# Kernel tuning notes

Hardware: AMD Instinct MI355X
Metric: run time of the kernel (lower is better)

Reference implementation:

```python
import jax, jax.numpy as jnp
import numpy as np

EXPERTS, IN_DIM, OUT_DIM, BATCH = 8, 1024, 1024, 16384

def setup_inputs() -> dict:
    key = jax.random.key(0)
    k1, k2, k3, k4 = jax.random.split(key, 4)
    bound = np.sqrt(6.0 / (IN_DIM * OUT_DIM)).astype(np.float32)
    bbound = np.sqrt(6.0 / (1 * OUT_DIM)).astype(np.float32)
    return {
        "x": jax.random.normal(k1, (BATCH, IN_DIM), dtype=jnp.float32),
        "weights": jax.random.uniform(k2, (BATCH, EXPERTS), dtype=jnp.float32),
        "W": jax.random.uniform(k3, (EXPERTS, IN_DIM, OUT_DIM), jnp.float32, -bound, bound),
        "b": jax.random.uniform(k4, (EXPERTS, 1, OUT_DIM), jnp.float32, -bbound, bbound),
    }

def reference(x, weights, W, b):
    # y[b,o] = sum_e weights[b,e] * (x[b,:] @ W[e] + b[e])
    # Fused triple einsum avoids materializing the [B,E,O] intermediate.
    y = jnp.einsum("be,bi,eio->bo", weights, x, W)
    y = y + jnp.einsum("be,eo->bo", weights, b[:, 0, :])
    return y
```

## Files before the change

### kernel.cpp

```cpp
#include <hip/hip_runtime.h>
#include <hip/hip_bf16.h>
#include <stdint.h>

#define BATCH   16384
#define EXPERTS 8
#define IN_DIM  1024
#define OUT_DIM 1024

typedef unsigned short u16;
typedef short  bf16x8 __attribute__((ext_vector_type(8)));
typedef float  f32x4  __attribute__((ext_vector_type(4)));

__device__ __forceinline__ u16 f2bf(float f) {
  uint32_t u = __float_as_uint(f);
  u += 0x7fffu + ((u >> 16) & 1u);
  return (u16)(u >> 16);
}

#define GLDS16(g, l)                                                      \
  __builtin_amdgcn_global_load_lds(                                       \
      (const __attribute__((address_space(1))) void*)(g),                 \
      (__attribute__((address_space(3))) void*)(l), 16, 0, 0)

#define MFMA_BF16 __builtin_amdgcn_mfma_f32_16x16x32_bf16
#define SB0 __builtin_amdgcn_sched_barrier(0)
#define LGKM(N) asm volatile("s_waitcnt lgkmcnt(" #N ")" ::: "memory")
#define VM0     asm volatile("s_waitcnt vmcnt(0)" ::: "memory")

__global__ void cvt_x(const float* __restrict__ x, u16* __restrict__ xb) {
  size_t i = ((size_t)blockIdx.x * 256 + threadIdx.x) * 4;
  float4 v = *reinterpret_cast<const float4*>(x + i);
  ushort4 o;
  o.x = f2bf(v.x); o.y = f2bf(v.y); o.z = f2bf(v.z); o.w = f2bf(v.w);
  *reinterpret_cast<ushort4*>(xb + i) = o;
}

__global__ void cvt_w(const float* __restrict__ W, u16* __restrict__ wbt) {
  __shared__ u16 t[64][72];
  const int e  = blockIdx.z;
  const int i0 = blockIdx.x * 64;
  const int o0 = blockIdx.y * 64;
  const int tid = threadIdx.x;
  const int c  = (tid & 15) * 4;
  const int r_ = tid >> 4;
  const float* src = W + ((size_t)e << 20);
#pragma unroll
  for (int p = 0; p < 4; ++p) {
    int r = r_ + p * 16;
    float4 v = *reinterpret_cast<const float4*>(src + (size_t)(i0 + r) * 1024 + o0 + c);
    t[r][c + 0] = f2bf(v.x); t[r][c + 1] = f2bf(v.y);
    t[r][c + 2] = f2bf(v.z); t[r][c + 3] = f2bf(v.w);
  }
  __syncthreads();
  u16* dst = wbt + ((size_t)e << 20);
#pragma unroll
  for (int p = 0; p < 4; ++p) {
    int orow = r_ + p * 16;
    ushort4 u;
    u.x = t[c + 0][orow]; u.y = t[c + 1][orow];
    u.z = t[c + 2][orow]; u.w = t[c + 3][orow];
    *reinterpret_cast<ushort4*>(dst + (size_t)(o0 + orow) * 1024 + i0 + c) = u;
  }
}

__global__ __launch_bounds__(512, 2)
void zgemm(const u16* __restrict__ xb, const u16* __restrict__ wbt,
           const float* __restrict__ wts, const float* __restrict__ bias,
           float* __restrict__ y) {
  __shared__ u16 sm[69632];
  char* smb = (char*)sm;
  float* rl = (float*)(sm + 65536);

  const int tid = threadIdx.x;
  const int l   = tid & 63;
  const int w   = tid >> 6;
  const int wm  = w >> 2;
  const int wn  = w & 3;
  const int x8  = blockIdx.x & 7;
  const int jj  = blockIdx.x >> 3;
  const int b0  = ((x8 << 3) + (jj >> 2)) << 8;
  const int n0  = (jj & 3) << 8;

#pragma unroll
  for (int i = 0; i < 4; ++i) {
    const int flat = tid + i * 512;
    const int e = flat & 7, r = flat >> 3;
    const float* wr = wts + (size_t)(b0 + r) * EXPERTS;
    float we = fmaxf(wr[e], 1e-20f);
    float rr = (e < 7) ? we / fmaxf(wr[e + 1], 1e-20f) : we;
    rl[e * 256 + r] = rr;
  }

  const int rbl   = (w << 3) + (l >> 3);
  const int chunk = ((l & 7) ^ (l >> 3)) << 3;
  const u16* pAg = xb  + (size_t)(b0 + rbl) * IN_DIM + chunk;
  const u16* pBg = wbt + (size_t)(n0 + rbl) * 1024 + chunk;

  const int l15  = l & 15;
  const int kb0  = (((l >> 4) << 4)) ^ ((l & 7) << 4);
  const int arow = (wm * 128 + l15) * 128;
  const int brow = (wn * 64 + l15) * 128;
  const int wlo  = (wm << 9) + ((l >> 4) << 4);

  f32x4 acc[8][4];
#pragma unroll
  for (int m = 0; m < 8; ++m)
#pragma unroll
    for (int n = 0; n < 4; ++n) acc[m][n] = (f32x4){0.f, 0.f, 0.f, 0.f};

#define STG_A(q, dstE, kv)                                                 \
  GLDS16(pAg + (size_t)((q) * 64) * 1024 + (size_t)(kv) * 64,              \
         sm + (dstE) + (q) * 4096 + (w << 9))
#define STG_B(q, dstE, off)                                                \
  GLDS16(pBg + (off) + (size_t)((q) * 64) * 1024,                          \
         sm + (dstE) + (q) * 4096 + (w << 9))

#define MM(AV, BV, MB)                                                     \
  __builtin_amdgcn_s_setprio(1);                                           \
  _Pragma("unroll")                                                        \
  for (int m = 0; m < 4; ++m)                                              \
    _Pragma("unroll")                                                      \
    for (int n = 0; n < 4; ++n)                                            \
      acc[(MB) + m][n] = MFMA_BF16(AV[m], BV[n], acc[(MB) + m][n], 0, 0, 0); \
  __builtin_amdgcn_s_setprio(0);

  STG_A(0, 0, 0); STG_A(1, 0, 0); STG_A(2, 0, 0); STG_A(3, 0, 0);
  STG_B(0, 32768, 0); STG_B(1, 32768, 0); STG_B(2, 32768, 0); STG_B(3, 32768, 0);
  VM0;
  LGKM(0);
  __builtin_amdgcn_s_barrier();

#define BODY(TT, ARB, BRB, AWE, BWE)                                       \
  {                                                                        \
    const int tn  = ((TT) + 1) & 127;                                      \
    const int e1  = tn >> 4, k1 = tn & 15;                                 \
    const size_t boffg = (size_t)e1 * 1048576 + (size_t)k1 * 64;           \
    bf16x8 a0[4], b0v[4], a1[4], a2v[4], b1v[4], a3[4];                    \
    _Pragma("unroll")                                                      \
    for (int m = 0; m < 4; ++m)                                            \
      a0[m] = *(const bf16x8*)(smb + (ARB) + arow + m * 2048 + kb0);       \
    _Pragma("unroll")                                                      \
    for (int n = 0; n < 4; ++n)                                            \
      b0v[n] = *(const bf16x8*)(smb + (BRB) + brow + n * 2048 + kb0);      \
    _Pragma("unroll")                                                      \
    for (int m = 0; m < 4; ++m)                                            \
      a1[m] = *(const bf16x8*)(smb + (ARB) + arow + (m + 4) * 2048 + kb0); \
    STG_A(0, AWE, k1); STG_A(1, AWE, k1); STG_A(2, AWE, k1); STG_A(3, AWE, k1); \
    STG_B(0, BWE, boffg); STG_B(1, BWE, boffg);                            \
    STG_B(2, BWE, boffg); STG_B(3, BWE, boffg);                            \
    LGKM(4); SB0;                              \
    _Pragma("unroll")                                                      \
    for (int m = 0; m < 4; ++m)                                            \
      a2v[m] = *(const bf16x8*)(smb + (ARB) + arow + m * 2048 + (kb0 ^ 64)); \
    _Pragma("unroll")                                                      \
    for (int n = 0; n < 4; ++n)                                            \
      b1v[n] = *(const bf16x8*)(smb + (BRB) + brow + n * 2048 + (kb0 ^ 64)); \
    MM(a0, b0v, 0)                                                 \
    LGKM(8); SB0;                                             \
    _Pragma("unroll")                                                      \
    for (int m = 0; m < 4; ++m)                                            \
      a3[m] = *(const bf16x8*)(smb + (ARB) + arow + (m + 4) * 2048 + (kb0 ^ 64)); \
    MM(a1, b0v, 4)                                                 \
    LGKM(4); SB0;                                             \
    MM(a2v, b1v, 0)                                                \
    LGKM(0); SB0;                                             \
    MM(a3, b1v, 4)                                                 \
    VM0;                                           \
    __builtin_amdgcn_s_barrier();              \
    if (((TT) & 15) == 15 && (TT) != 127) {                                \
      const int e = (TT) >> 4;                                             \
      f32x4 rv[8];                                                         \
      _Pragma("unroll")                                                    \
      for (int m = 0; m < 8; ++m)                                          \
        rv[m] = *(const f32x4*)(smb + 131072 + e * 1024 + wlo + m * 64);   \
      LGKM(0); SB0;                                                        \
      _Pragma("unroll")                                                    \
      for (int m = 0; m < 8; ++m)                                          \
        _Pragma("unroll")                                                  \
        for (int n = 0; n < 4; ++n) acc[m][n] *= rv[m];                    \
    }                                                                      \
  }

#pragma unroll 1
  for (int t = 0; t < 128; t += 2) {
    BODY(t,     0,     65536, 16384, 49152)
    BODY(t + 1, 32768, 98304, 0,     32768)
  }
  VM0; LGKM(0);

  float bv[4][8];
#pragma unroll
  for (int n = 0; n < 4; ++n) {
    const int c = n0 + wn * 64 + n * 16 + l15;
#pragma unroll
    for (int ee = 0; ee < 8; ++ee) bv[n][ee] = bias[ee * OUT_DIM + c];
  }
#pragma unroll
  for (int m = 0; m < 8; ++m) {
    const f32x4 rv7 = *(const f32x4*)(smb + 131072 + 7 * 1024 + wlo + m * 64);
    const int r0 = b0 + wm * 128 + m * 16 + ((l >> 4) << 2);
#pragma unroll
    for (int j = 0; j < 4; ++j) {
      const float* wr = wts + (size_t)(r0 + j) * EXPERTS;
      float w8[8];
#pragma unroll
      for (int ee = 0; ee < 8; ++ee) w8[ee] = wr[ee];
#pragma unroll
      for (int n = 0; n < 4; ++n) {
        const int c = n0 + wn * 64 + n * 16 + l15;
        float v = acc[m][n][j] * rv7[j];
#pragma unroll
        for (int ee = 0; ee < 8; ++ee) v += w8[ee] * bv[n][ee];
        y[(size_t)(r0 + j) * OUT_DIM + c] = v;
      }
    }
  }
}

extern "C" void kernel_launch(void* const* d_in, const int* in_sizes, int n_in,
                              void* d_out, int out_size, void* d_ws, size_t ws_size,
                              hipStream_t stream) {
  const float* x    = (const float*)d_in[0];
  const float* wts  = (const float*)d_in[1];
  const float* W    = (const float*)d_in[2];
  const float* bias = (const float*)d_in[3];
  float* y = (float*)d_out;

  const size_t xb_elems = (size_t)BATCH * IN_DIM;
  const size_t wb_elems = (size_t)EXPERTS * IN_DIM * OUT_DIM;
  if (ws_size < (xb_elems + wb_elems) * sizeof(u16)) return;
  u16* xb  = (u16*)d_ws;
  u16* wbt = xb + xb_elems;

  cvt_x<<<(BATCH * IN_DIM) / (4 * 256), 256, 0, stream>>>(x, xb);
  cvt_w<<<dim3(IN_DIM / 64, OUT_DIM / 64, EXPERTS), 256, 0, stream>>>(W, wbt);
  zgemm<<<dim3(256), 512, 0, stream>>>(xb, wbt, wts, bias, y);
}
```

Measured before the change: 243.8 us.

## Switch main GEMM from 16x16x32 to 32x32x16 bf16 MFMA tiles

Replaces the 16x16x32 MFMA with 32x32x16 MFMA, regrouping each warp's 128x64 tile into 4x2 blocks of 32x32 accumulators. This changes the LDS fragment reads (fewer B reads per k-step) and the per-expert rescale and epilogue index mapping. The epilogue also loads the eight routing weights with two float4 loads instead of scalar loads. The intent is to cut LDS traffic and instruction count per FLOP, at the cost of a different LDS-wait schedule and new swizzle and index arithmetic that must still line up with the staging layout.

```diff
diff --git a/kernel.cpp b/kernel.cpp
--- a/kernel.cpp
+++ b/kernel.cpp
@@ -10,6 +10,7 @@
 typedef unsigned short u16;
 typedef short  bf16x8 __attribute__((ext_vector_type(8)));
 typedef float  f32x4  __attribute__((ext_vector_type(4)));
+typedef float  f32x16 __attribute__((ext_vector_type(16)));
 
 __device__ __forceinline__ u16 f2bf(float f) {
   uint32_t u = __float_as_uint(f);
@@ -22,7 +23,7 @@
       (const __attribute__((address_space(1))) void*)(g),                 \
       (__attribute__((address_space(3))) void*)(l), 16, 0, 0)
 
-#define MFMA_BF16 __builtin_amdgcn_mfma_f32_16x16x32_bf16
+#define MFMA32 __builtin_amdgcn_mfma_f32_32x32x16_bf16
 #define SB0 __builtin_amdgcn_sched_barrier(0)
 #define LGKM(N) asm volatile("s_waitcnt lgkmcnt(" #N ")" ::: "memory")
 #define VM0     asm volatile("s_waitcnt vmcnt(0)" ::: "memory")
@@ -96,17 +97,19 @@
   const u16* pAg = xb  + (size_t)(b0 + rbl) * IN_DIM + chunk;
   const u16* pBg = wbt + (size_t)(n0 + rbl) * 1024 + chunk;
 
-  const int l15  = l & 15;
-  const int kb0  = (((l >> 4) << 4)) ^ ((l & 7) << 4);
-  const int arow = (wm * 128 + l15) * 128;
-  const int brow = (wn * 64 + l15) * 128;
-  const int wlo  = (wm << 9) + ((l >> 4) << 4);
-
-  f32x4 acc[8][4];
-#pragma unroll
-  for (int m = 0; m < 8; ++m)
-#pragma unroll
-    for (int n = 0; n < 4; ++n) acc[m][n] = (f32x4){0.f, 0.f, 0.f, 0.f};
+  const int l31   = l & 31;
+  const int kb0   = ((l >> 5) << 4) ^ ((l & 7) << 4);
+  const int arow2 = (wm * 128 + l31) * 128;
+  const int brow2 = (wn * 64 + l31) * 128;
+  const int wlo2  = (wm << 9) + ((l >> 5) << 4);
+
+  f32x16 acc[4][2];
+#pragma unroll
+  for (int mb = 0; mb < 4; ++mb)
+#pragma unroll
+    for (int nb = 0; nb < 2; ++nb)
+#pragma unroll
+      for (int j = 0; j < 16; ++j) acc[mb][nb][j] = 0.f;
 
 #define STG_A(q, dstE, kv)                                                 \
   GLDS16(pAg + (size_t)((q) * 64) * 1024 + (size_t)(kv) * 64,              \
@@ -115,13 +118,21 @@
   GLDS16(pBg + (off) + (size_t)((q) * 64) * 1024,                          \
          sm + (dstE) + (q) * 4096 + (w << 9))
 
-#define MM(AV, BV, MB)                                                     \
+#define RDF(AS, BS, KB, ARB, BRB)                                          \
+    _Pragma("unroll")                                                      \
+    for (int mb = 0; mb < 4; ++mb)                                         \
+      AS[mb] = *(const bf16x8*)(smb + (ARB) + arow2 + mb * 4096 + (KB));   \
+    _Pragma("unroll")                                                      \
+    for (int nb = 0; nb < 2; ++nb)                                         \
+      BS[nb] = *(const bf16x8*)(smb + (BRB) + brow2 + nb * 4096 + (KB));
+
+#define MM32(AV, BV)                                                       \
   __builtin_amdgcn_s_setprio(1);                                           \
   _Pragma("unroll")                                                        \
-  for (int m = 0; m < 4; ++m)                                              \
+  for (int mb = 0; mb < 4; ++mb)                                           \
     _Pragma("unroll")                                                      \
-    for (int n = 0; n < 4; ++n)                                            \
-      acc[(MB) + m][n] = MFMA_BF16(AV[m], BV[n], acc[(MB) + m][n], 0, 0, 0); \
+    for (int nb = 0; nb < 2; ++nb)                                         \
+      acc[mb][nb] = MFMA32(AV[mb], BV[nb], acc[mb][nb], 0, 0, 0);          \
   __builtin_amdgcn_s_setprio(0);
 
   STG_A(0, 0, 0); STG_A(1, 0, 0); STG_A(2, 0, 0); STG_A(3, 0, 0);
@@ -135,49 +146,43 @@
     const int tn  = ((TT) + 1) & 127;                                      \
     const int e1  = tn >> 4, k1 = tn & 15;                                 \
     const size_t boffg = (size_t)e1 * 1048576 + (size_t)k1 * 64;           \
-    bf16x8 a0[4], b0v[4], a1[4], a2v[4], b1v[4], a3[4];                    \
-    _Pragma("unroll")                                                      \
-    for (int m = 0; m < 4; ++m)                                            \
-      a0[m] = *(const bf16x8*)(smb + (ARB) + arow + m * 2048 + kb0);       \
-    _Pragma("unroll")                                                      \
-    for (int n = 0; n < 4; ++n)                                            \
-      b0v[n] = *(const bf16x8*)(smb + (BRB) + brow + n * 2048 + kb0);      \
-    _Pragma("unroll")                                                      \
-    for (int m = 0; m < 4; ++m)                                            \
-      a1[m] = *(const bf16x8*)(smb + (ARB) + arow + (m + 4) * 2048 + kb0); \
+    bf16x8 A0[4], B0[2], A1[4], B1[2], A2[4], B2[2], A3[4], B3[2];         \
+    RDF(A0, B0, kb0,      ARB, BRB)                                        \
+    RDF(A1, B1, kb0 ^ 32, ARB, BRB)                                        \
     STG_A(0, AWE, k1); STG_A(1, AWE, k1); STG_A(2, AWE, k1); STG_A(3, AWE, k1); \
     STG_B(0, BWE, boffg); STG_B(1, BWE, boffg);                            \
     STG_B(2, BWE, boffg); STG_B(3, BWE, boffg);                            \
-    LGKM(4); SB0;                              \
-    _Pragma("unroll")                                                      \
-    for (int m = 0; m < 4; ++m)                                            \
-      a2v[m] = *(const bf16x8*)(smb + (ARB) + arow + m * 2048 + (kb0 ^ 64)); \
-    _Pragma("unroll")                                                      \
-    for (int n = 0; n < 4; ++n)                                            \
-      b1v[n] = *(const bf16x8*)(smb + (BRB) + brow + n * 2048 + (kb0 ^ 64)); \
-    MM(a0, b0v, 0)                                                 \
-    LGKM(8); SB0;                                             \
-    _Pragma("unroll")                                                      \
-    for (int m = 0; m < 4; ++m)                                            \
-      a3[m] = *(const bf16x8*)(smb + (ARB) + arow + (m + 4) * 2048 + (kb0 ^ 64)); \
-    MM(a1, b0v, 4)                                                 \
-    LGKM(4); SB0;                                             \
-    MM(a2v, b1v, 0)                                                \
+    LGKM(6); SB0;                              \
+    RDF(A2, B2, kb0 ^ 64, ARB, BRB)                                        \
+    MM32(A0, B0)                                                   \
+    LGKM(6); SB0;                                             \
+    RDF(A3, B3, kb0 ^ 96, ARB, BRB)                                        \
+    MM32(A1, B1)                                                   \
+    LGKM(6); SB0;                                             \
+    MM32(A2, B2)                                                   \
     LGKM(0); SB0;                                             \
-    MM(a3, b1v, 4)                                                 \
+    MM32(A3, B3)                                                   \
     VM0;                                           \
     __builtin_amdgcn_s_barrier();              \
     if (((TT) & 15) == 15 && (TT) != 127) {                                \
       const int e = (TT) >> 4;                                             \
-      f32x4 rv[8];                                                         \
+      f32x4 rv[4][4];                                                      \
       _Pragma("unroll")                                                    \
-      for (int m = 0; m < 8; ++m)                                          \
-        rv[m] = *(const f32x4*)(smb + 131072 + e * 1024 + wlo + m * 64);   \
+      for (int mb = 0; mb < 4; ++mb)                                       \
+        _Pragma("unroll")                                                  \
+        for (int q = 0; q < 4; ++q)                                        \
+          rv[mb][q] = *(const f32x4*)(smb + 131072 + e * 1024 + wlo2       \
+                                      + mb * 128 + q * 32);                \
       LGKM(0); SB0;                                                        \
       _Pragma("unroll")                                                    \
-      for (int m = 0; m < 8; ++m)                                          \
+      for (int mb = 0; mb < 4; ++mb)                                       \
         _Pragma("unroll")                                                  \
-        for (int n = 0; n < 4; ++n) acc[m][n] *= rv[m];                    \
+        for (int nb = 0; nb < 2; ++nb)                                     \
+          _Pragma("unroll")                                                \
+          for (int q = 0; q < 4; ++q)                                      \
+            _Pragma("unroll")                                              \
+            for (int j = 0; j < 4; ++j)                                    \
+              acc[mb][nb][4 * q + j] *= rv[mb][q][j];                      \
     }                                                                      \
   }
 
@@ -188,30 +193,36 @@
   }
   VM0; LGKM(0);
 
-  float bv[4][8];
-#pragma unroll
-  for (int n = 0; n < 4; ++n) {
-    const int c = n0 + wn * 64 + n * 16 + l15;
-#pragma unroll
-    for (int ee = 0; ee < 8; ++ee) bv[n][ee] = bias[ee * OUT_DIM + c];
-  }
-#pragma unroll
-  for (int m = 0; m < 8; ++m) {
-    const f32x4 rv7 = *(const f32x4*)(smb + 131072 + 7 * 1024 + wlo + m * 64);
-    const int r0 = b0 + wm * 128 + m * 16 + ((l >> 4) << 2);
-#pragma unroll
-    for (int j = 0; j < 4; ++j) {
-      const float* wr = wts + (size_t)(r0 + j) * EXPERTS;
-      float w8[8];
-#pragma unroll
-      for (int ee = 0; ee < 8; ++ee) w8[ee] = wr[ee];
-#pragma unroll
-      for (int n = 0; n < 4; ++n) {
-        const int c = n0 + wn * 64 + n * 16 + l15;
-        float v = acc[m][n][j] * rv7[j];
-#pragma unroll
-        for (int ee = 0; ee < 8; ++ee) v += w8[ee] * bv[n][ee];
-        y[(size_t)(r0 + j) * OUT_DIM + c] = v;
+  float bv[2][8];
+#pragma unroll
+  for (int nb = 0; nb < 2; ++nb) {
+    const int c = n0 + wn * 64 + nb * 32 + l31;
+#pragma unroll
+    for (int ee = 0; ee < 8; ++ee) bv[nb][ee] = bias[ee * OUT_DIM + c];
+  }
+#pragma unroll
+  for (int mb = 0; mb < 4; ++mb) {
+    f32x4 rv7[4];
+#pragma unroll
+    for (int q = 0; q < 4; ++q)
+      rv7[q] = *(const f32x4*)(smb + 131072 + 7 * 1024 + wlo2 + mb * 128 + q * 32);
+#pragma unroll
+    for (int q = 0; q < 4; ++q) {
+      const int rbase = b0 + wm * 128 + mb * 32 + q * 8 + ((l >> 5) << 2);
+#pragma unroll
+      for (int j = 0; j < 4; ++j) {
+        const int row = rbase + j;
+        float4 wl4 = *reinterpret_cast<const float4*>(wts + (size_t)row * 8);
+        float4 wh4 = *reinterpret_cast<const float4*>(wts + (size_t)row * 8 + 4);
+        float w8[8] = {wl4.x, wl4.y, wl4.z, wl4.w, wh4.x, wh4.y, wh4.z, wh4.w};
+#pragma unroll
+        for (int nb = 0; nb < 2; ++nb) {
+          const int c = n0 + wn * 64 + nb * 32 + l31;
+          float v = acc[mb][nb][4 * q + j] * rv7[q][j];
+#pragma unroll
+          for (int ee = 0; ee < 8; ++ee) v += w8[ee] * bv[nb][ee];
+          y[(size_t)row * OUT_DIM + c] = v;
+        }
       }
     }
   }
```

New measurement: 279.2 us. 14.6% more time.
